# Optimization experiments

Hardware: AMD Instinct MI355X
Metric: run time of the kernel (lower is better)

## Reference

```python
import jax, jax.numpy as jnp
import numpy as np

N = 40000
E = 640000
IN_F, HID, OUT_F = 128, 128, 64


def setup_inputs() -> dict:
    key = jax.random.key(0)
    ks = jax.random.split(key, 6)
    x = jax.random.normal(ks[0], (N, IN_F), dtype=jnp.float32)
    edge_index = jax.random.randint(ks[1], (2, E), 0, N, dtype=jnp.int64)
    s_in = 1.0 / np.sqrt(IN_F)
    s_hid = 1.0 / np.sqrt(HID)
    W1l = jax.random.normal(ks[2], (IN_F, HID), dtype=jnp.float32) * s_in
    W1r = jax.random.normal(ks[3], (IN_F, HID), dtype=jnp.float32) * s_in
    b1 = jnp.zeros((HID,), dtype=jnp.float32)
    W2l = jax.random.normal(ks[4], (HID, OUT_F), dtype=jnp.float32) * s_hid
    W2r = jax.random.normal(ks[5], (HID, OUT_F), dtype=jnp.float32) * s_hid
    b2 = jnp.zeros((OUT_F,), dtype=jnp.float32)
    return {"x": x, "edge_index": edge_index, "W1l": W1l, "b1": b1,
            "W1r": W1r, "W2l": W2l, "b2": b2, "W2r": W2r}


def _mean_agg(x, src, dst, n_nodes):
    # mean of source-node features over incoming edges at each destination
    sums = jax.ops.segment_sum(x[src], dst, num_segments=n_nodes)  # [N, D]
    cnt = jax.ops.segment_sum(jnp.ones((src.shape[0],), x.dtype), dst,
                              num_segments=n_nodes)
    return sums / jnp.maximum(cnt, 1.0)[:, None]


def _sage_conv(x, src, dst, Wl, b, Wr, n_nodes):
    # PyG SAGEConv (mean aggr): lin_l(mean_j x_j) + lin_r(x_i), bias in lin_l
    agg = _mean_agg(x, src, dst, n_nodes)
    return agg @ Wl + b + x @ Wr


def reference(x, edge_index, W1l, b1, W1r, W2l, b2, W2r):
    src, dst = edge_index[0], edge_index[1]
    n = x.shape[0]
    h = jax.nn.relu(_sage_conv(x, src, dst, W1l, b1, W1r, n))
    return _sage_conv(h, src, dst, W2l, b2, W2r, n)
```

## Files before the change

### kernel.cpp

```cpp
#include <hip/hip_runtime.h>

#define NNODES 40000
#define NEDGES 640000
#define PAD 64
#define NBK 160
#define BNODES 250
#define BCAP 8192
#define ACHUNK 4000

typedef unsigned int uint32;
typedef unsigned short ushort16;
typedef short bf16x8 __attribute__((ext_vector_type(8)));
typedef float f32x4 __attribute__((ext_vector_type(4)));

static __device__ __forceinline__ ushort16 f2bf(float f) {
    uint32 u = __builtin_bit_cast(uint32, f);
    uint32 r = u + 0x7fffu + ((u >> 16) & 1u);
    return (ushort16)(r >> 16);
}
static __device__ __forceinline__ float bf_lo(uint32 u) {
    uint32 t = u << 16;
    return __builtin_bit_cast(float, t);
}
static __device__ __forceinline__ float bf_hi(uint32 u) {
    uint32 t = u & 0xffff0000u;
    return __builtin_bit_cast(float, t);
}

static __device__ __forceinline__ void acc8(float* s, uint4 u) {
    s[0] += bf_lo(u.x); s[1] += bf_hi(u.x);
    s[2] += bf_lo(u.y); s[3] += bf_hi(u.y);
    s[4] += bf_lo(u.z); s[5] += bf_hi(u.z);
    s[6] += bf_lo(u.w); s[7] += bf_hi(u.w);
}

static __device__ __forceinline__ int edge_val(const void* ep, long long idx, int is64) {
    if (is64) return (int)((const long long*)ep)[idx];
    return ((const int*)ep)[idx];
}

static __device__ __forceinline__ int imin(int a, int b) { return a < b ? a : b; }

__global__ void prep_kernel(const float* __restrict__ x, uint32* __restrict__ xbf2,
                            int* __restrict__ gcur,
                            const float* __restrict__ W1l, const float* __restrict__ W1r,
                            const float* __restrict__ W2l, const float* __restrict__ W2r,
                            ushort16* __restrict__ Wfrag1, ushort16* __restrict__ Wfrag2,
                            const int* __restrict__ e32, int* __restrict__ flag) {
    int b = blockIdx.x;
    if (b < 5000) {
        int i = b * 256 + threadIdx.x;
        float4 v = ((const float4*)x)[i];
        uint2 o;
        o.x = (uint32)f2bf(v.x) | ((uint32)f2bf(v.y) << 16);
        o.y = (uint32)f2bf(v.z) | ((uint32)f2bf(v.w) << 16);
        ((uint2*)xbf2)[i] = o;
        return;
    }
    int i = (b - 5000) * 256 + threadIdx.x;
    if (i < NBK) gcur[i] = 0;
    if (i == 0) {
        int any = 0;
        for (int t = 0; t < 64; ++t) any |= e32[2 * t + 1];
        *flag = (any == 0) ? 1 : 0;
    }
    if (i < 32768) {
        int j = i & 7, lane = (i >> 3) & 63, nt = (i >> 9) & 7, s = (i >> 12) & 3, by = i >> 14;
        int k = s * 32 + (lane >> 4) * 8 + j;
        int col = nt * 16 + (lane & 15);
        float v = (by == 0) ? W1l[k * 128 + col] : W1r[k * 128 + col];
        Wfrag1[i] = f2bf(v);
    } else {
        int q = i - 32768;
        int j = q & 7, lane = (q >> 3) & 63, nt = (q >> 9) & 7, s = (q >> 12) & 3;
        int k = s * 32 + (lane >> 4) * 8 + j;
        int col = nt * 16 + (lane & 15);
        float v = (col < 64) ? W2l[k * 64 + col] : W2r[k * 64 + (col - 64)];
        Wfrag2[q] = f2bf(v);
    }
}

__global__ __launch_bounds__(256) void buildA_kernel(const void* __restrict__ edges,
                                                     const int* __restrict__ flag,
                                                     int* __restrict__ gcur,
                                                     int* __restrict__ bstream) {
    __shared__ int hist[NBK];
    __shared__ int cur[NBK];
    int tid = threadIdx.x;
    int base = blockIdx.x * ACHUNK;
    for (int i = tid; i < NBK; i += 256) hist[i] = 0;
    __syncthreads();
    int is64 = *flag;
#pragma unroll
    for (int k = 0; k < (ACHUNK + 255) / 256; ++k) {
        int off = k * 256 + tid;
        if (off < ACHUNK) {
            int d = edge_val(edges, (long long)NEDGES + base + off, is64);
            atomicAdd(&hist[d / BNODES], 1);
        }
    }
    __syncthreads();
    if (tid < NBK) cur[tid] = atomicAdd(&gcur[tid], hist[tid]);
    __syncthreads();
#pragma unroll
    for (int k = 0; k < (ACHUNK + 255) / 256; ++k) {
        int off = k * 256 + tid;
        if (off < ACHUNK) {
            int e = base + off;
            int d = edge_val(edges, (long long)NEDGES + e, is64);
            int s = edge_val(edges, e, is64);
            int bk = d / BNODES;
            int dloc = d - bk * BNODES;
            int r = atomicAdd(&cur[bk], 1);
            if (r < BCAP) bstream[bk * BCAP + r] = (s << 8) | dloc;
        }
    }
}

__global__ __launch_bounds__(256) void buildB_kernel(const int* __restrict__ bstream,
                                                     const int* __restrict__ gcur,
                                                     int* __restrict__ cnt,
                                                     int* __restrict__ csr_src) {
    __shared__ int4 img4[BNODES * 16];
    __shared__ int hist[BNODES];
    int* img = (int*)img4;
    int tid = threadIdx.x;
    int bk = blockIdx.x;
    for (int i = tid; i < BNODES; i += 256) hist[i] = 0;
    __syncthreads();
    int n = gcur[bk];
    if (n > BCAP) n = BCAP;
    for (int i = tid; i < n; i += 256) {
        int u = bstream[bk * BCAP + i];
        int dloc = u & 255;
        int s = u >> 8;
        int r = atomicAdd(&hist[dloc], 1);
        if (r < PAD) img[dloc * PAD + r] = s;
    }
    __syncthreads();
    int4* csr4 = (int4*)csr_src;
#pragma unroll
    for (int i = tid; i < BNODES * 16; i += 256) csr4[(size_t)bk * BNODES * 16 + i] = img4[i];
    for (int i = tid; i < BNODES; i += 256) cnt[bk * BNODES + i] = hist[i];
}

__global__ __launch_bounds__(256) void gemm_mfma_kernel(const ushort16* __restrict__ Abf,
                                                        const uint4* __restrict__ WfragG,
                                                        int Lw, int Rw,
                                                        ushort16* __restrict__ bfL,
                                                        ushort16* __restrict__ bfR,
                                                        float* __restrict__ fR) {
    __shared__ uint4 Bs[2048];
    int tid = threadIdx.x;
#pragma unroll
    for (int it = 0; it < 8; ++it) {
        int idx = tid + it * 256;
        Bs[idx] = WfragG[(size_t)blockIdx.y * 2048 + idx];
    }

    int wv = tid >> 6, lane = tid & 63;
    int quad = lane >> 4, c = lane & 15;
    int row0 = blockIdx.x * 64 + wv * 16;

    const uint4* arow = (const uint4*)(Abf + (size_t)(row0 + c) * 128);
    bf16x8 af[4];
#pragma unroll
    for (int s = 0; s < 4; ++s) af[s] = __builtin_bit_cast(bf16x8, arow[s * 4 + quad]);

    __syncthreads();

    f32x4 acc[8];
#pragma unroll
    for (int nt = 0; nt < 8; ++nt) acc[nt] = (f32x4){0.f, 0.f, 0.f, 0.f};

#pragma unroll
    for (int s = 0; s < 4; ++s) {
#pragma unroll
        for (int nt = 0; nt < 8; ++nt) {
            bf16x8 bf = __builtin_bit_cast(bf16x8, Bs[(s * 8 + nt) * 64 + lane]);
            acc[nt] = __builtin_amdgcn_mfma_f32_16x16x32_bf16(af[s], bf, acc[nt], 0, 0, 0);
        }
    }

    int colbase = blockIdx.y * 128;
#pragma unroll
    for (int nt = 0; nt < 8; ++nt) {
        int gcol = colbase + nt * 16 + c;
#pragma unroll
        for (int r = 0; r < 4; ++r) {
            int row = row0 + quad * 4 + r;
            if (gcol < Lw) {
                bfL[(size_t)row * Lw + gcol] = f2bf(acc[nt][r]);
            } else if (bfR) {
                bfR[(size_t)row * Rw + (gcol - Lw)] = f2bf(acc[nt][r]);
            } else {
                fR[(size_t)row * Rw + (gcol - Lw)] = acc[nt][r];
            }
        }
    }
}

__global__ __launch_bounds__(256) void agg1_kernel(const uint4* __restrict__ P4,
                                                   const uint4* __restrict__ S4,
                                                   const int* __restrict__ cnt,
                                                   const int* __restrict__ csr_src,
                                                   const float* __restrict__ b1,
                                                   uint4* __restrict__ hbf4) {
    int wave = threadIdx.x >> 6, lane = threadIdx.x & 63;
    int node = blockIdx.x * 4 + wave;
    if (node >= NNODES) return;
    int c = cnt[node];
    if (c > PAD) c = PAD;
    int beg = node * PAD;
    int sub = lane >> 4;
    int fl = lane & 15;
    float s[8];
#pragma unroll
    for (int i = 0; i < 8; ++i) s[i] = 0.f;

    int idx = csr_src[beg + lane];
    int cm1 = c - 1;
    for (int e = 0; e < c; e += 16) {
        int e0 = e + sub, e1 = e + 4 + sub, e2 = e + 8 + sub, e3 = e + 12 + sub;
        int a0 = __shfl(idx, imin(e0, cm1));
        int a1 = __shfl(idx, imin(e1, cm1));
        int a2 = __shfl(idx, imin(e2, cm1));
        int a3 = __shfl(idx, imin(e3, cm1));
        uint4 u0 = P4[(size_t)a0 * 16 + fl];
        uint4 u1 = P4[(size_t)a1 * 16 + fl];
        uint4 u2 = P4[(size_t)a2 * 16 + fl];
        uint4 u3 = P4[(size_t)a3 * 16 + fl];
        if (e0 < c) acc8(s, u0);
        if (e1 < c) acc8(s, u1);
        if (e2 < c) acc8(s, u2);
        if (e3 < c) acc8(s, u3);
    }
#pragma unroll
    for (int i = 0; i < 8; ++i) s[i] += __shfl_xor(s[i], 16);
#pragma unroll
    for (int i = 0; i < 8; ++i) s[i] += __shfl_xor(s[i], 32);

    if (sub == 0) {
        float ic = 1.0f / (float)(c > 0 ? c : 1);
        uint4 su = S4[(size_t)node * 16 + fl];
        float4 bA = *(const float4*)&b1[fl * 8];
        float4 bB = *(const float4*)&b1[fl * 8 + 4];
        float sv[8];
        sv[0] = bf_lo(su.x); sv[1] = bf_hi(su.x);
        sv[2] = bf_lo(su.y); sv[3] = bf_hi(su.y);
        sv[4] = bf_lo(su.z); sv[5] = bf_hi(su.z);
        sv[6] = bf_lo(su.w); sv[7] = bf_hi(su.w);
        float bb[8] = {bA.x, bA.y, bA.z, bA.w, bB.x, bB.y, bB.z, bB.w};
        float v[8];
#pragma unroll
        for (int i = 0; i < 8; ++i) v[i] = fmaxf(fmaf(s[i], ic, bb[i] + sv[i]), 0.f);
        uint4 o;
        o.x = (uint32)f2bf(v[0]) | ((uint32)f2bf(v[1]) << 16);
        o.y = (uint32)f2bf(v[2]) | ((uint32)f2bf(v[3]) << 16);
        o.z = (uint32)f2bf(v[4]) | ((uint32)f2bf(v[5]) << 16);
        o.w = (uint32)f2bf(v[6]) | ((uint32)f2bf(v[7]) << 16);
        hbf4[(size_t)node * 16 + fl] = o;
    }
}

__global__ __launch_bounds__(256) void agg2_kernel(const uint4* __restrict__ P4,
                                                   const float* __restrict__ selfR2,
                                                   const int* __restrict__ cnt,
                                                   const int* __restrict__ csr_src,
                                                   const float* __restrict__ b2,
                                                   float* __restrict__ out) {
    int wave = threadIdx.x >> 6, lane = threadIdx.x & 63;
    int node = blockIdx.x * 4 + wave;
    if (node >= NNODES) return;
    int c = cnt[node];
    if (c > PAD) c = PAD;
    int beg = node * PAD;
    int sub = lane >> 3;
    int fl = lane & 7;
    float s[8];
#pragma unroll
    for (int i = 0; i < 8; ++i) s[i] = 0.f;

    int idx = csr_src[beg + lane];
    int cm1 = c - 1;
    for (int e = 0; e < c; e += 32) {
        int e0 = e + sub, e1 = e + 8 + sub, e2 = e + 16 + sub, e3 = e + 24 + sub;
        int a0 = __shfl(idx, imin(e0, cm1));
        int a1 = __shfl(idx, imin(e1, cm1));
        int a2 = __shfl(idx, imin(e2, cm1));
        int a3 = __shfl(idx, imin(e3, cm1));
        uint4 u0 = P4[(size_t)a0 * 8 + fl];
        uint4 u1 = P4[(size_t)a1 * 8 + fl];
        uint4 u2 = P4[(size_t)a2 * 8 + fl];
        uint4 u3 = P4[(size_t)a3 * 8 + fl];
        if (e0 < c) acc8(s, u0);
        if (e1 < c) acc8(s, u1);
        if (e2 < c) acc8(s, u2);
        if (e3 < c) acc8(s, u3);
    }
#pragma unroll
    for (int i = 0; i < 8; ++i) s[i] += __shfl_xor(s[i], 8);
#pragma unroll
    for (int i = 0; i < 8; ++i) s[i] += __shfl_xor(s[i], 16);
#pragma unroll
    for (int i = 0; i < 8; ++i) s[i] += __shfl_xor(s[i], 32);

    if (sub == 0) {
        float ic = 1.0f / (float)(c > 0 ? c : 1);
        float4 sA = *(const float4*)&selfR2[(size_t)node * 64 + fl * 8];
        float4 sB = *(const float4*)&selfR2[(size_t)node * 64 + fl * 8 + 4];
        float4 bA = *(const float4*)&b2[fl * 8];
        float4 bB = *(const float4*)&b2[fl * 8 + 4];
        float sv[8] = {sA.x, sA.y, sA.z, sA.w, sB.x, sB.y, sB.z, sB.w};
        float bb[8] = {bA.x, bA.y, bA.z, bA.w, bB.x, bB.y, bB.z, bB.w};
        float v[8];
#pragma unroll
        for (int i = 0; i < 8; ++i) v[i] = fmaf(s[i], ic, bb[i] + sv[i]);
        float4 o0 = make_float4(v[0], v[1], v[2], v[3]);
        float4 o1 = make_float4(v[4], v[5], v[6], v[7]);
        *(float4*)&out[(size_t)node * 64 + fl * 8] = o0;
        *(float4*)&out[(size_t)node * 64 + fl * 8 + 4] = o1;
    }
}

extern "C" void kernel_launch(void* const* d_in, const int* in_sizes, int n_in,
                              void* d_out, int out_size, void* d_ws, size_t ws_size,
                              hipStream_t stream) {
    const float* x   = (const float*)d_in[0];
    const void*  ei  = d_in[1];
    const float* W1l = (const float*)d_in[2];
    const float* b1  = (const float*)d_in[3];
    const float* W1r = (const float*)d_in[4];
    const float* W2l = (const float*)d_in[5];
    const float* b2  = (const float*)d_in[6];
    const float* W2r = (const float*)d_in[7];
    float* out = (float*)d_out;

    char* p = (char*)d_ws;
    auto alloc = [&](size_t bytes) {
        char* r = p;
        p += (bytes + 255) & ~(size_t)255;
        return r;
    };
    int*      flag      = (int*)alloc(4);
    int*      cnt       = (int*)alloc(NNODES * 4);
    int*      gcur      = (int*)alloc(NBK * 4);
    int*      bstream   = (int*)alloc((size_t)NBK * BCAP * 4);
    int*      csr_src   = (int*)alloc((size_t)NNODES * PAD * 4);
    ushort16* Wfrag1    = (ushort16*)alloc(32768 * 2);
    ushort16* Wfrag2    = (ushort16*)alloc(16384 * 2);
    uint32*   xbf       = (uint32*)alloc((size_t)NNODES * 64 * 4);
    ushort16* T1l       = (ushort16*)alloc((size_t)NNODES * 128 * 2);
    ushort16* T1r       = (ushort16*)alloc((size_t)NNODES * 128 * 2);
    uint32*   hbf       = (uint32*)alloc((size_t)NNODES * 64 * 4);
    ushort16* T2l       = (ushort16*)alloc((size_t)NNODES * 64 * 2);
    float*    T2r       = (float*)alloc((size_t)NNODES * 64 * 4);

    prep_kernel<<<5192, 256, 0, stream>>>(x, xbf, gcur, W1l, W1r, W2l, W2r, Wfrag1, Wfrag2,
                                          (const int*)ei, flag);
    buildA_kernel<<<NBK, 256, 0, stream>>>(ei, flag, gcur, bstream);
    buildB_kernel<<<NBK, 256, 0, stream>>>(bstream, gcur, cnt, csr_src);

    gemm_mfma_kernel<<<dim3(NNODES / 64, 2), 256, 0, stream>>>(
        (const ushort16*)xbf, (const uint4*)Wfrag1, 128, 128, T1l, T1r, (float*)nullptr);
    agg1_kernel<<<(NNODES + 3) / 4, 256, 0, stream>>>((const uint4*)T1l, (const uint4*)T1r,
                                                      cnt, csr_src, b1, (uint4*)hbf);

    gemm_mfma_kernel<<<dim3(NNODES / 64, 1), 256, 0, stream>>>(
        (const ushort16*)hbf, (const uint4*)Wfrag2, 64, 64, T2l, (ushort16*)nullptr, T2r);
    agg2_kernel<<<(NNODES + 3) / 4, 256, 0, stream>>>((const uint4*)T2l, T2r, cnt, csr_src, b2,
                                                      out);
}
```

Baseline: 173.0 us.

## Split feature tables into 32-column chunks and use 16-bit CSR indices

Feature matrices (x in bf16, the GEMM left outputs, and the hidden activations) are stored as 32-column chunk-major planes. The aggregation kernels gain a grid dimension over those chunks, so each gather touches a smaller, more cache-resident table and the number of node-waves grows. CSR source indices are stored as 16-bit values, halving index storage and traffic. In exchange, each neighbor index is loaded and shuffled once per chunk rather than once per node. The 16-bit index only holds because node ids fit in 16 bits, which is true for the fixed 40000-node graph.

```diff
diff --git a/kernel.cpp b/kernel.cpp
--- a/kernel.cpp
+++ b/kernel.cpp
@@ -50,11 +50,13 @@
     int b = blockIdx.x;
     if (b < 5000) {
         int i = b * 256 + threadIdx.x;
+        int row = i >> 5, j = i & 31;
         float4 v = ((const float4*)x)[i];
         uint2 o;
         o.x = (uint32)f2bf(v.x) | ((uint32)f2bf(v.y) << 16);
         o.y = (uint32)f2bf(v.z) | ((uint32)f2bf(v.w) << 16);
-        ((uint2*)xbf2)[i] = o;
+        int chunk = j >> 3, cj = j & 7;
+        ((uint2*)xbf2)[((size_t)chunk * NNODES + row) * 8 + cj] = o;
         return;
     }
     int i = (b - 5000) * 256 + threadIdx.x;
@@ -120,10 +122,10 @@
 __global__ __launch_bounds__(256) void buildB_kernel(const int* __restrict__ bstream,
                                                      const int* __restrict__ gcur,
                                                      int* __restrict__ cnt,
-                                                     int* __restrict__ csr_src) {
-    __shared__ int4 img4[BNODES * 16];
+                                                     unsigned short* __restrict__ csr16) {
+    __shared__ uint4 img4[BNODES * 8];
     __shared__ int hist[BNODES];
-    int* img = (int*)img4;
+    unsigned short* img = (unsigned short*)img4;
     int tid = threadIdx.x;
     int bk = blockIdx.x;
     for (int i = tid; i < BNODES; i += 256) hist[i] = 0;
@@ -133,18 +135,17 @@
     for (int i = tid; i < n; i += 256) {
         int u = bstream[bk * BCAP + i];
         int dloc = u & 255;
-        int s = u >> 8;
         int r = atomicAdd(&hist[dloc], 1);
-        if (r < PAD) img[dloc * PAD + r] = s;
-    }
-    __syncthreads();
-    int4* csr4 = (int4*)csr_src;
-#pragma unroll
-    for (int i = tid; i < BNODES * 16; i += 256) csr4[(size_t)bk * BNODES * 16 + i] = img4[i];
+        if (r < PAD) img[dloc * PAD + r] = (unsigned short)(u >> 8);
+    }
+    __syncthreads();
+    uint4* dst = (uint4*)(csr16 + (size_t)bk * BNODES * PAD);
+#pragma unroll
+    for (int i = tid; i < BNODES * 8; i += 256) dst[i] = img4[i];
     for (int i = tid; i < BNODES; i += 256) cnt[bk * BNODES + i] = hist[i];
 }
 
-__global__ __launch_bounds__(256) void gemm_mfma_kernel(const ushort16* __restrict__ Abf,
+__global__ __launch_bounds__(256) void gemm_mfma_kernel(const uint4* __restrict__ Achunk,
                                                         const uint4* __restrict__ WfragG,
                                                         int Lw, int Rw,
                                                         ushort16* __restrict__ bfL,
@@ -162,10 +163,10 @@
     int quad = lane >> 4, c = lane & 15;
     int row0 = blockIdx.x * 64 + wv * 16;
 
-    const uint4* arow = (const uint4*)(Abf + (size_t)(row0 + c) * 128);
     bf16x8 af[4];
 #pragma unroll
-    for (int s = 0; s < 4; ++s) af[s] = __builtin_bit_cast(bf16x8, arow[s * 4 + quad]);
+    for (int s = 0; s < 4; ++s)
+        af[s] = __builtin_bit_cast(bf16x8, Achunk[((size_t)s * NNODES + row0 + c) * 4 + quad]);
 
     __syncthreads();
 
@@ -190,7 +191,7 @@
         for (int r = 0; r < 4; ++r) {
             int row = row0 + quad * 4 + r;
             if (gcol < Lw) {
-                bfL[(size_t)row * Lw + gcol] = f2bf(acc[nt][r]);
+                bfL[((size_t)(gcol >> 5) * NNODES + row) * 32 + (gcol & 31)] = f2bf(acc[nt][r]);
             } else if (bfR) {
                 bfR[(size_t)row * Rw + (gcol - Lw)] = f2bf(acc[nt][r]);
             } else {
@@ -200,41 +201,39 @@
     }
 }
 
-__global__ __launch_bounds__(256) void agg1_kernel(const uint4* __restrict__ P4,
+__global__ __launch_bounds__(256) void agg1_kernel(const uint4* __restrict__ P4c,
                                                    const uint4* __restrict__ S4,
                                                    const int* __restrict__ cnt,
-                                                   const int* __restrict__ csr_src,
+                                                   const unsigned short* __restrict__ csr16,
                                                    const float* __restrict__ b1,
-                                                   uint4* __restrict__ hbf4) {
+                                                   uint4* __restrict__ hbf4c) {
     int wave = threadIdx.x >> 6, lane = threadIdx.x & 63;
     int node = blockIdx.x * 4 + wave;
-    if (node >= NNODES) return;
+    int y = blockIdx.y;
     int c = cnt[node];
     if (c > PAD) c = PAD;
-    int beg = node * PAD;
-    int sub = lane >> 4;
-    int fl = lane & 15;
+    int sub = lane >> 2;
+    int fl = lane & 3;
     float s[8];
 #pragma unroll
     for (int i = 0; i < 8; ++i) s[i] = 0.f;
 
-    int idx = csr_src[beg + lane];
+    int idx = csr16[(size_t)node * PAD + lane];
     int cm1 = c - 1;
-    for (int e = 0; e < c; e += 16) {
-        int e0 = e + sub, e1 = e + 4 + sub, e2 = e + 8 + sub, e3 = e + 12 + sub;
+    const uint4* T = P4c + (size_t)y * NNODES * 4;
+    for (int e = 0; e < c; e += 32) {
+        int e0 = e + sub, e1 = e + 16 + sub;
         int a0 = __shfl(idx, imin(e0, cm1));
         int a1 = __shfl(idx, imin(e1, cm1));
-        int a2 = __shfl(idx, imin(e2, cm1));
-        int a3 = __shfl(idx, imin(e3, cm1));
-        uint4 u0 = P4[(size_t)a0 * 16 + fl];
-        uint4 u1 = P4[(size_t)a1 * 16 + fl];
-        uint4 u2 = P4[(size_t)a2 * 16 + fl];
-        uint4 u3 = P4[(size_t)a3 * 16 + fl];
+        uint4 u0 = T[(size_t)a0 * 4 + fl];
+        uint4 u1 = T[(size_t)a1 * 4 + fl];
         if (e0 < c) acc8(s, u0);
         if (e1 < c) acc8(s, u1);
-        if (e2 < c) acc8(s, u2);
-        if (e3 < c) acc8(s, u3);
-    }
+    }
+#pragma unroll
+    for (int i = 0; i < 8; ++i) s[i] += __shfl_xor(s[i], 4);
+#pragma unroll
+    for (int i = 0; i < 8; ++i) s[i] += __shfl_xor(s[i], 8);
 #pragma unroll
     for (int i = 0; i < 8; ++i) s[i] += __shfl_xor(s[i], 16);
 #pragma unroll
@@ -242,9 +241,10 @@
 
     if (sub == 0) {
         float ic = 1.0f / (float)(c > 0 ? c : 1);
-        uint4 su = S4[(size_t)node * 16 + fl];
-        float4 bA = *(const float4*)&b1[fl * 8];
-        float4 bB = *(const float4*)&b1[fl * 8 + 4];
+        uint4 su = S4[(size_t)node * 16 + y * 4 + fl];
+        const float* bp = &b1[y * 32 + fl * 8];
+        float4 bA = *(const float4*)bp;
+        float4 bB = *(const float4*)(bp + 4);
         float sv[8];
         sv[0] = bf_lo(su.x); sv[1] = bf_hi(su.x);
         sv[2] = bf_lo(su.y); sv[3] = bf_hi(su.y);
@@ -259,45 +259,41 @@
         o.y = (uint32)f2bf(v[2]) | ((uint32)f2bf(v[3]) << 16);
         o.z = (uint32)f2bf(v[4]) | ((uint32)f2bf(v[5]) << 16);
         o.w = (uint32)f2bf(v[6]) | ((uint32)f2bf(v[7]) << 16);
-        hbf4[(size_t)node * 16 + fl] = o;
-    }
-}
-
-__global__ __launch_bounds__(256) void agg2_kernel(const uint4* __restrict__ P4,
+        hbf4c[((size_t)y * NNODES + node) * 4 + fl] = o;
+    }
+}
+
+__global__ __launch_bounds__(256) void agg2_kernel(const uint4* __restrict__ P4c,
                                                    const float* __restrict__ selfR2,
                                                    const int* __restrict__ cnt,
-                                                   const int* __restrict__ csr_src,
+                                                   const unsigned short* __restrict__ csr16,
                                                    const float* __restrict__ b2,
                                                    float* __restrict__ out) {
     int wave = threadIdx.x >> 6, lane = threadIdx.x & 63;
     int node = blockIdx.x * 4 + wave;
-    if (node >= NNODES) return;
+    int y = blockIdx.y;
     int c = cnt[node];
     if (c > PAD) c = PAD;
-    int beg = node * PAD;
-    int sub = lane >> 3;
-    int fl = lane & 7;
+    int sub = lane >> 2;
+    int fl = lane & 3;
     float s[8];
 #pragma unroll
     for (int i = 0; i < 8; ++i) s[i] = 0.f;
 
-    int idx = csr_src[beg + lane];
+    int idx = csr16[(size_t)node * PAD + lane];
     int cm1 = c - 1;
+    const uint4* T = P4c + (size_t)y * NNODES * 4;
     for (int e = 0; e < c; e += 32) {
-        int e0 = e + sub, e1 = e + 8 + sub, e2 = e + 16 + sub, e3 = e + 24 + sub;
+        int e0 = e + sub, e1 = e + 16 + sub;
         int a0 = __shfl(idx, imin(e0, cm1));
         int a1 = __shfl(idx, imin(e1, cm1));
-        int a2 = __shfl(idx, imin(e2, cm1));
-        int a3 = __shfl(idx, imin(e3, cm1));
-        uint4 u0 = P4[(size_t)a0 * 8 + fl];
-        uint4 u1 = P4[(size_t)a1 * 8 + fl];
-        uint4 u2 = P4[(size_t)a2 * 8 + fl];
-        uint4 u3 = P4[(size_t)a3 * 8 + fl];
+        uint4 u0 = T[(size_t)a0 * 4 + fl];
+        uint4 u1 = T[(size_t)a1 * 4 + fl];
         if (e0 < c) acc8(s, u0);
         if (e1 < c) acc8(s, u1);
-        if (e2 < c) acc8(s, u2);
-        if (e3 < c) acc8(s, u3);
-    }
+    }
+#pragma unroll
+    for (int i = 0; i < 8; ++i) s[i] += __shfl_xor(s[i], 4);
 #pragma unroll
     for (int i = 0; i < 8; ++i) s[i] += __shfl_xor(s[i], 8);
 #pragma unroll
@@ -307,19 +303,20 @@
 
     if (sub == 0) {
         float ic = 1.0f / (float)(c > 0 ? c : 1);
-        float4 sA = *(const float4*)&selfR2[(size_t)node * 64 + fl * 8];
-        float4 sB = *(const float4*)&selfR2[(size_t)node * 64 + fl * 8 + 4];
-        float4 bA = *(const float4*)&b2[fl * 8];
-        float4 bB = *(const float4*)&b2[fl * 8 + 4];
+        const float* sp = &selfR2[(size_t)node * 64 + y * 32 + fl * 8];
+        float4 sA = *(const float4*)sp;
+        float4 sB = *(const float4*)(sp + 4);
+        const float* bp = &b2[y * 32 + fl * 8];
+        float4 bA = *(const float4*)bp;
+        float4 bB = *(const float4*)(bp + 4);
         float sv[8] = {sA.x, sA.y, sA.z, sA.w, sB.x, sB.y, sB.z, sB.w};
         float bb[8] = {bA.x, bA.y, bA.z, bA.w, bB.x, bB.y, bB.z, bB.w};
         float v[8];
 #pragma unroll
         for (int i = 0; i < 8; ++i) v[i] = fmaf(s[i], ic, bb[i] + sv[i]);
-        float4 o0 = make_float4(v[0], v[1], v[2], v[3]);
-        float4 o1 = make_float4(v[4], v[5], v[6], v[7]);
-        *(float4*)&out[(size_t)node * 64 + fl * 8] = o0;
-        *(float4*)&out[(size_t)node * 64 + fl * 8 + 4] = o1;
+        float* op = &out[(size_t)node * 64 + y * 32 + fl * 8];
+        *(float4*)op = make_float4(v[0], v[1], v[2], v[3]);
+        *(float4*)(op + 4) = make_float4(v[4], v[5], v[6], v[7]);
     }
 }
 
@@ -342,32 +339,32 @@
         p += (bytes + 255) & ~(size_t)255;
         return r;
     };
-    int*      flag      = (int*)alloc(4);
-    int*      cnt       = (int*)alloc(NNODES * 4);
-    int*      gcur      = (int*)alloc(NBK * 4);
-    int*      bstream   = (int*)alloc((size_t)NBK * BCAP * 4);
-    int*      csr_src   = (int*)alloc((size_t)NNODES * PAD * 4);
-    ushort16* Wfrag1    = (ushort16*)alloc(32768 * 2);
-    ushort16* Wfrag2    = (ushort16*)alloc(16384 * 2);
-    uint32*   xbf       = (uint32*)alloc((size_t)NNODES * 64 * 4);
-    ushort16* T1l       = (ushort16*)alloc((size_t)NNODES * 128 * 2);
-    ushort16* T1r       = (ushort16*)alloc((size_t)NNODES * 128 * 2);
-    uint32*   hbf       = (uint32*)alloc((size_t)NNODES * 64 * 4);
-    ushort16* T2l       = (ushort16*)alloc((size_t)NNODES * 64 * 2);
-    float*    T2r       = (float*)alloc((size_t)NNODES * 64 * 4);
+    int*            flag    = (int*)alloc(4);
+    int*            cnt     = (int*)alloc(NNODES * 4);
+    int*            gcur    = (int*)alloc(NBK * 4);
+    int*            bstream = (int*)alloc((size_t)NBK * BCAP * 4);
+    unsigned short* csr16   = (unsigned short*)alloc((size_t)NNODES * PAD * 2);
+    ushort16*       Wfrag1  = (ushort16*)alloc(32768 * 2);
+    ushort16*       Wfrag2  = (ushort16*)alloc(16384 * 2);
+    uint32*         xbf     = (uint32*)alloc((size_t)NNODES * 64 * 4);
+    ushort16*       T1l     = (ushort16*)alloc((size_t)NNODES * 128 * 2);
+    ushort16*       T1r     = (ushort16*)alloc((size_t)NNODES * 128 * 2);
+    uint32*         hbf     = (uint32*)alloc((size_t)NNODES * 64 * 4);
+    ushort16*       T2l     = (ushort16*)alloc((size_t)NNODES * 64 * 2);
+    float*          T2r     = (float*)alloc((size_t)NNODES * 64 * 4);
 
     prep_kernel<<<5192, 256, 0, stream>>>(x, xbf, gcur, W1l, W1r, W2l, W2r, Wfrag1, Wfrag2,
                                           (const int*)ei, flag);
     buildA_kernel<<<NBK, 256, 0, stream>>>(ei, flag, gcur, bstream);
-    buildB_kernel<<<NBK, 256, 0, stream>>>(bstream, gcur, cnt, csr_src);
+    buildB_kernel<<<NBK, 256, 0, stream>>>(bstream, gcur, cnt, csr16);
 
     gemm_mfma_kernel<<<dim3(NNODES / 64, 2), 256, 0, stream>>>(
-        (const ushort16*)xbf, (const uint4*)Wfrag1, 128, 128, T1l, T1r, (float*)nullptr);
-    agg1_kernel<<<(NNODES + 3) / 4, 256, 0, stream>>>((const uint4*)T1l, (const uint4*)T1r,
-                                                      cnt, csr_src, b1, (uint4*)hbf);
+        (const uint4*)xbf, (const uint4*)Wfrag1, 128, 128, T1l, T1r, (float*)nullptr);
+    agg1_kernel<<<dim3(NNODES / 4, 4), 256, 0, stream>>>((const uint4*)T1l, (const uint4*)T1r,
+                                                         cnt, csr16, b1, (uint4*)hbf);
 
     gemm_mfma_kernel<<<dim3(NNODES / 64, 1), 256, 0, stream>>>(
-        (const ushort16*)hbf, (const uint4*)Wfrag2, 64, 64, T2l, (ushort16*)nullptr, T2r);
-    agg2_kernel<<<(NNODES + 3) / 4, 256, 0, stream>>>((const uint4*)T2l, T2r, cnt, csr_src, b2,
-                                                      out);
-}
+        (const uint4*)hbf, (const uint4*)Wfrag2, 64, 64, T2l, (ushort16*)nullptr, T2r);
+    agg2_kernel<<<dim3(NNODES / 4, 2), 256, 0, stream>>>((const uint4*)T2l, T2r, cnt, csr16,
+                                                         b2, out);
+}
```

After: 223.2 us. 1.29x slower.

## Fuse edge bucketing into prep kernel with per-workgroup slots and 16-bit CSR

Applied to the files above, without the earlier changes.

Merges the bucketing pass into the prep kernel. Each workgroup now writes edges into its own fixed-capacity slot per bucket, so the global histogram pass and global atomics go away and one launch is saved. The CSR source indices are stored as 16-bit values, halving the CSR image traffic in the build and aggregation kernels. The risks are that node IDs up to 40000 fit 16 bits only because N < 65536, and edges are silently dropped if a workgroup/bucket pair exceeds 80 entries (the mean is 25). buildB also scans a sparse 160x80 slot grid.

```diff
diff --git a/kernel.cpp b/kernel.cpp
--- a/kernel.cpp
+++ b/kernel.cpp
@@ -5,7 +5,7 @@
 #define PAD 64
 #define NBK 160
 #define BNODES 250
-#define BCAP 8192
+#define SCAP 80
 #define ACHUNK 4000
 
 typedef unsigned int uint32;
@@ -41,15 +41,18 @@
 
 static __device__ __forceinline__ int imin(int a, int b) { return a < b ? a : b; }
 
-__global__ void prep_kernel(const float* __restrict__ x, uint32* __restrict__ xbf2,
-                            int* __restrict__ gcur,
-                            const float* __restrict__ W1l, const float* __restrict__ W1r,
-                            const float* __restrict__ W2l, const float* __restrict__ W2r,
-                            ushort16* __restrict__ Wfrag1, ushort16* __restrict__ Wfrag2,
-                            const int* __restrict__ e32, int* __restrict__ flag) {
+__global__ void prep_build_kernel(const float* __restrict__ x, uint32* __restrict__ xbf2,
+                                  const float* __restrict__ W1l, const float* __restrict__ W1r,
+                                  const float* __restrict__ W2l, const float* __restrict__ W2r,
+                                  ushort16* __restrict__ Wfrag1, ushort16* __restrict__ Wfrag2,
+                                  const void* __restrict__ edges, const int* __restrict__ e32,
+                                  int* __restrict__ bstream, int* __restrict__ wgcnt) {
+    __shared__ int lcnt[NBK];
+    __shared__ int s_is64;
     int b = blockIdx.x;
+    int tid = threadIdx.x;
     if (b < 5000) {
-        int i = b * 256 + threadIdx.x;
+        int i = b * 256 + tid;
         float4 v = ((const float4*)x)[i];
         uint2 o;
         o.x = (uint32)f2bf(v.x) | ((uint32)f2bf(v.y) << 16);
@@ -57,51 +60,35 @@
         ((uint2*)xbf2)[i] = o;
         return;
     }
-    int i = (b - 5000) * 256 + threadIdx.x;
-    if (i < NBK) gcur[i] = 0;
-    if (i == 0) {
+    if (b < 5192) {
+        int i = (b - 5000) * 256 + tid;
+        if (i < 32768) {
+            int j = i & 7, lane = (i >> 3) & 63, nt = (i >> 9) & 7, s = (i >> 12) & 3,
+                by = i >> 14;
+            int k = s * 32 + (lane >> 4) * 8 + j;
+            int col = nt * 16 + (lane & 15);
+            float v = (by == 0) ? W1l[k * 128 + col] : W1r[k * 128 + col];
+            Wfrag1[i] = f2bf(v);
+        } else {
+            int q = i - 32768;
+            int j = q & 7, lane = (q >> 3) & 63, nt = (q >> 9) & 7, s = (q >> 12) & 3;
+            int k = s * 32 + (lane >> 4) * 8 + j;
+            int col = nt * 16 + (lane & 15);
+            float v = (col < 64) ? W2l[k * 64 + col] : W2r[k * 64 + (col - 64)];
+            Wfrag2[q] = f2bf(v);
+        }
+        return;
+    }
+    int wg = b - 5192;
+    for (int i = tid; i < NBK; i += 256) lcnt[i] = 0;
+    if (tid == 0) {
         int any = 0;
         for (int t = 0; t < 64; ++t) any |= e32[2 * t + 1];
-        *flag = (any == 0) ? 1 : 0;
-    }
-    if (i < 32768) {
-        int j = i & 7, lane = (i >> 3) & 63, nt = (i >> 9) & 7, s = (i >> 12) & 3, by = i >> 14;
-        int k = s * 32 + (lane >> 4) * 8 + j;
-        int col = nt * 16 + (lane & 15);
-        float v = (by == 0) ? W1l[k * 128 + col] : W1r[k * 128 + col];
-        Wfrag1[i] = f2bf(v);
-    } else {
-        int q = i - 32768;
-        int j = q & 7, lane = (q >> 3) & 63, nt = (q >> 9) & 7, s = (q >> 12) & 3;
-        int k = s * 32 + (lane >> 4) * 8 + j;
-        int col = nt * 16 + (lane & 15);
-        float v = (col < 64) ? W2l[k * 64 + col] : W2r[k * 64 + (col - 64)];
-        Wfrag2[q] = f2bf(v);
-    }
-}
-
-__global__ __launch_bounds__(256) void buildA_kernel(const void* __restrict__ edges,
-                                                     const int* __restrict__ flag,
-                                                     int* __restrict__ gcur,
-                                                     int* __restrict__ bstream) {
-    __shared__ int hist[NBK];
-    __shared__ int cur[NBK];
-    int tid = threadIdx.x;
-    int base = blockIdx.x * ACHUNK;
-    for (int i = tid; i < NBK; i += 256) hist[i] = 0;
-    __syncthreads();
-    int is64 = *flag;
-#pragma unroll
-    for (int k = 0; k < (ACHUNK + 255) / 256; ++k) {
-        int off = k * 256 + tid;
-        if (off < ACHUNK) {
-            int d = edge_val(edges, (long long)NEDGES + base + off, is64);
-            atomicAdd(&hist[d / BNODES], 1);
-        }
-    }
-    __syncthreads();
-    if (tid < NBK) cur[tid] = atomicAdd(&gcur[tid], hist[tid]);
-    __syncthreads();
+        s_is64 = (any == 0) ? 1 : 0;
+    }
+    __syncthreads();
+    int is64 = s_is64;
+    int base = wg * ACHUNK;
 #pragma unroll
     for (int k = 0; k < (ACHUNK + 255) / 256; ++k) {
         int off = k * 256 + tid;
@@ -111,36 +98,39 @@
             int s = edge_val(edges, e, is64);
             int bk = d / BNODES;
             int dloc = d - bk * BNODES;
-            int r = atomicAdd(&cur[bk], 1);
-            if (r < BCAP) bstream[bk * BCAP + r] = (s << 8) | dloc;
-        }
-    }
+            int r = atomicAdd(&lcnt[bk], 1);
+            if (r < SCAP) bstream[(bk * NBK + wg) * SCAP + r] = (s << 8) | dloc;
+        }
+    }
+    __syncthreads();
+    for (int i = tid; i < NBK; i += 256) wgcnt[wg * NBK + i] = imin(lcnt[i], SCAP);
 }
 
 __global__ __launch_bounds__(256) void buildB_kernel(const int* __restrict__ bstream,
-                                                     const int* __restrict__ gcur,
+                                                     const int* __restrict__ wgcnt,
                                                      int* __restrict__ cnt,
-                                                     int* __restrict__ csr_src) {
-    __shared__ int4 img4[BNODES * 16];
+                                                     unsigned short* __restrict__ csr16) {
+    __shared__ uint4 img4[BNODES * 8];
     __shared__ int hist[BNODES];
-    int* img = (int*)img4;
+    unsigned short* img = (unsigned short*)img4;
     int tid = threadIdx.x;
     int bk = blockIdx.x;
     for (int i = tid; i < BNODES; i += 256) hist[i] = 0;
     __syncthreads();
-    int n = gcur[bk];
-    if (n > BCAP) n = BCAP;
-    for (int i = tid; i < n; i += 256) {
-        int u = bstream[bk * BCAP + i];
-        int dloc = u & 255;
-        int s = u >> 8;
-        int r = atomicAdd(&hist[dloc], 1);
-        if (r < PAD) img[dloc * PAD + r] = s;
-    }
-    __syncthreads();
-    int4* csr4 = (int4*)csr_src;
-#pragma unroll
-    for (int i = tid; i < BNODES * 16; i += 256) csr4[(size_t)bk * BNODES * 16 + i] = img4[i];
+    for (int i = tid; i < NBK * SCAP; i += 256) {
+        int wg = i / SCAP;
+        int r = i - wg * SCAP;
+        if (r < wgcnt[wg * NBK + bk]) {
+            int u = bstream[(bk * NBK + wg) * SCAP + r];
+            int dloc = u & 255;
+            int rr = atomicAdd(&hist[dloc], 1);
+            if (rr < PAD) img[dloc * PAD + rr] = (unsigned short)(u >> 8);
+        }
+    }
+    __syncthreads();
+    uint4* dst = (uint4*)(csr16 + (size_t)bk * BNODES * PAD);
+#pragma unroll
+    for (int i = tid; i < BNODES * 8; i += 256) dst[i] = img4[i];
     for (int i = tid; i < BNODES; i += 256) cnt[bk * BNODES + i] = hist[i];
 }
 
@@ -203,7 +193,7 @@
 __global__ __launch_bounds__(256) void agg1_kernel(const uint4* __restrict__ P4,
                                                    const uint4* __restrict__ S4,
                                                    const int* __restrict__ cnt,
-                                                   const int* __restrict__ csr_src,
+                                                   const unsigned short* __restrict__ csr16,
                                                    const float* __restrict__ b1,
                                                    uint4* __restrict__ hbf4) {
     int wave = threadIdx.x >> 6, lane = threadIdx.x & 63;
@@ -211,14 +201,13 @@
     if (node >= NNODES) return;
     int c = cnt[node];
     if (c > PAD) c = PAD;
-    int beg = node * PAD;
     int sub = lane >> 4;
     int fl = lane & 15;
     float s[8];
 #pragma unroll
     for (int i = 0; i < 8; ++i) s[i] = 0.f;
 
-    int idx = csr_src[beg + lane];
+    int idx = csr16[(size_t)node * PAD + lane];
     int cm1 = c - 1;
     for (int e = 0; e < c; e += 16) {
         int e0 = e + sub, e1 = e + 4 + sub, e2 = e + 8 + sub, e3 = e + 12 + sub;
@@ -266,7 +255,7 @@
 __global__ __launch_bounds__(256) void agg2_kernel(const uint4* __restrict__ P4,
                                                    const float* __restrict__ selfR2,
                                                    const int* __restrict__ cnt,
-                                                   const int* __restrict__ csr_src,
+                                                   const unsigned short* __restrict__ csr16,
                                                    const float* __restrict__ b2,
                                                    float* __restrict__ out) {
     int wave = threadIdx.x >> 6, lane = threadIdx.x & 63;
@@ -274,14 +263,13 @@
     if (node >= NNODES) return;
     int c = cnt[node];
     if (c > PAD) c = PAD;
-    int beg = node * PAD;
     int sub = lane >> 3;
     int fl = lane & 7;
     float s[8];
 #pragma unroll
     for (int i = 0; i < 8; ++i) s[i] = 0.f;
 
-    int idx = csr_src[beg + lane];
+    int idx = csr16[(size_t)node * PAD + lane];
     int cm1 = c - 1;
     for (int e = 0; e < c; e += 32) {
         int e0 = e + sub, e1 = e + 8 + sub, e2 = e + 16 + sub, e3 = e + 24 + sub;
@@ -342,32 +330,30 @@
         p += (bytes + 255) & ~(size_t)255;
         return r;
     };
-    int*      flag      = (int*)alloc(4);
-    int*      cnt       = (int*)alloc(NNODES * 4);
-    int*      gcur      = (int*)alloc(NBK * 4);
-    int*      bstream   = (int*)alloc((size_t)NBK * BCAP * 4);
-    int*      csr_src   = (int*)alloc((size_t)NNODES * PAD * 4);
-    ushort16* Wfrag1    = (ushort16*)alloc(32768 * 2);
-    ushort16* Wfrag2    = (ushort16*)alloc(16384 * 2);
-    uint32*   xbf       = (uint32*)alloc((size_t)NNODES * 64 * 4);
-    ushort16* T1l       = (ushort16*)alloc((size_t)NNODES * 128 * 2);
-    ushort16* T1r       = (ushort16*)alloc((size_t)NNODES * 128 * 2);
-    uint32*   hbf       = (uint32*)alloc((size_t)NNODES * 64 * 4);
-    ushort16* T2l       = (ushort16*)alloc((size_t)NNODES * 64 * 2);
-    float*    T2r       = (float*)alloc((size_t)NNODES * 64 * 4);
-
-    prep_kernel<<<5192, 256, 0, stream>>>(x, xbf, gcur, W1l, W1r, W2l, W2r, Wfrag1, Wfrag2,
-                                          (const int*)ei, flag);
-    buildA_kernel<<<NBK, 256, 0, stream>>>(ei, flag, gcur, bstream);
-    buildB_kernel<<<NBK, 256, 0, stream>>>(bstream, gcur, cnt, csr_src);
+    int*            cnt     = (int*)alloc(NNODES * 4);
+    int*            wgcnt   = (int*)alloc((size_t)NBK * NBK * 4);
+    int*            bstream = (int*)alloc((size_t)NBK * NBK * SCAP * 4);
+    unsigned short* csr16   = (unsigned short*)alloc((size_t)NNODES * PAD * 2);
+    ushort16*       Wfrag1  = (ushort16*)alloc(32768 * 2);
+    ushort16*       Wfrag2  = (ushort16*)alloc(16384 * 2);
+    uint32*         xbf     = (uint32*)alloc((size_t)NNODES * 64 * 4);
+    ushort16*       T1l     = (ushort16*)alloc((size_t)NNODES * 128 * 2);
+    ushort16*       T1r     = (ushort16*)alloc((size_t)NNODES * 128 * 2);
+    uint32*         hbf     = (uint32*)alloc((size_t)NNODES * 64 * 4);
+    ushort16*       T2l     = (ushort16*)alloc((size_t)NNODES * 64 * 2);
+    float*          T2r     = (float*)alloc((size_t)NNODES * 64 * 4);
+
+    prep_build_kernel<<<5352, 256, 0, stream>>>(x, xbf, W1l, W1r, W2l, W2r, Wfrag1, Wfrag2,
+                                                ei, (const int*)ei, bstream, wgcnt);
+    buildB_kernel<<<NBK, 256, 0, stream>>>(bstream, wgcnt, cnt, csr16);
 
     gemm_mfma_kernel<<<dim3(NNODES / 64, 2), 256, 0, stream>>>(
         (const ushort16*)xbf, (const uint4*)Wfrag1, 128, 128, T1l, T1r, (float*)nullptr);
     agg1_kernel<<<(NNODES + 3) / 4, 256, 0, stream>>>((const uint4*)T1l, (const uint4*)T1r,
-                                                      cnt, csr_src, b1, (uint4*)hbf);
+                                                      cnt, csr16, b1, (uint4*)hbf);
 
     gemm_mfma_kernel<<<dim3(NNODES / 64, 1), 256, 0, stream>>>(
         (const ushort16*)hbf, (const uint4*)Wfrag2, 64, 64, T2l, (ushort16*)nullptr, T2r);
-    agg2_kernel<<<(NNODES + 3) / 4, 256, 0, stream>>>((const uint4*)T2l, T2r, cnt, csr_src, b2,
+    agg2_kernel<<<(NNODES + 3) / 4, 256, 0, stream>>>((const uint4*)T2l, T2r, cnt, csr16, b2,
                                                       out);
 }
```

After: 189.3 us. +9.4%, slower.
